# Optimization experiments

Measured on AMD Instinct MI355X. Metric: run time of the kernel, lower is better.

The kernel has to match this reference:

```python
import jax, jax.numpy as jnp
import numpy as np

B = 65536
NUM_INPUTS = 128
H0, H1 = 512, 512
K = 200
MIN_W = 0.001
MIN_H = 0.001
MIN_D = 0.001
EDGE_CONST = float(np.log(np.exp(1.0 - 0.001) - 1.0))  # in-place edge derivative value
LN_EPS = 1e-5


def setup_inputs() -> dict:
    key = jax.random.key(0)
    ks = jax.random.split(key, 10)
    f32 = jnp.float32
    inputs = jax.random.normal(ks[0], (B, NUM_INPUTS), dtype=f32)
    W1 = jax.random.normal(ks[1], (H0, NUM_INPUTS), dtype=f32) / np.sqrt(NUM_INPUTS)
    b1 = jnp.zeros((H0,), f32)
    g1 = jnp.ones((H0,), f32)
    be1 = jnp.zeros((H0,), f32)
    W2 = jax.random.normal(ks[2], (H1, H0), dtype=f32) / np.sqrt(H0)
    b2 = jnp.zeros((H1,), f32)
    g2 = jnp.ones((H1,), f32)
    be2 = jnp.zeros((H1,), f32)
    WV = jax.random.normal(ks[3], (3 * K - 1, H1), dtype=f32) / np.sqrt(H1)
    bV = jnp.zeros((3 * K - 1,), f32)
    Wa = jax.random.normal(ks[4], (1, H1), dtype=f32) / np.sqrt(H1)
    ba = jnp.zeros((1,), f32)
    Wb = jax.random.normal(ks[5], (1, H1), dtype=f32) / np.sqrt(H1)
    bb = jnp.zeros((1,), f32)
    return {"inputs": inputs, "W1": W1, "b1": b1, "g1": g1, "be1": be1,
            "W2": W2, "b2": b2, "g2": g2, "be2": be2,
            "WV": WV, "bV": bV, "Wa": Wa, "ba": ba, "Wb": Wb, "bb": bb}


def _layernorm(x, g, b):
    m = jnp.mean(x, axis=-1, keepdims=True)
    v = jnp.mean(jnp.square(x - m), axis=-1, keepdims=True)
    return (x - m) * jax.lax.rsqrt(v + LN_EPS) * g + b


def _spline_forward(inputs, W1, b1, g1, be1, W2, b2, g2, be2, WV, bV, Wa, ba, Wb, bb):
    x = jax.nn.relu(_layernorm(inputs @ W1.T + b1, g1, be1))
    x = jax.nn.relu(_layernorm(x @ W2.T + b2, g2, be2))
    sp = x @ WV.T + bV                      # [B, 3K-1]
    scale_a = jnp.exp(x @ Wa.T + ba)        # [B, 1]
    scale_b = x @ Wb.T + bb                 # [B, 1]

    Wp = jax.nn.softmax(sp[:, :K], axis=1)
    Hp = jax.nn.softmax(sp[:, K:2 * K], axis=1)
    Dp = sp[:, 2 * K:]                      # [B, K-1]
    Wp = MIN_W + (1.0 - MIN_W * K) * Wp
    Hp = MIN_H + (1.0 - MIN_H * K) * Hp
    Dp = MIN_D + jax.nn.softplus(Dp)
    bsz = inputs.shape[0]
    edge = jnp.full((bsz, 1), EDGE_CONST, dtype=inputs.dtype)
    D = jnp.concatenate([edge, Dp, edge], axis=-1)          # [B, K+1]

    zero = jnp.zeros((bsz, 1), dtype=inputs.dtype)
    cw = jnp.concatenate([zero, jnp.cumsum(Wp, axis=-1)], axis=-1)
    cw = cw.at[:, -1].set(1.0)                              # [B, K+1]
    widths = cw[:, 1:] - cw[:, :-1]                         # [B, K]
    ch = jnp.concatenate([zero, jnp.cumsum(Hp, axis=-1)], axis=-1)
    ch = scale_a * ch + scale_b                             # [B, K+1]
    heights = ch[:, 1:] - ch[:, :-1]                        # [B, K]

    tau = ((jnp.arange(K, dtype=inputs.dtype) + 0.5) / K)   # [K]
    tau = jnp.broadcast_to(tau, (bsz, K))

    # sum(tau >= bins) - 1 == searchsorted(bins, tau, side='right') - 1
    bin_idx = jax.vmap(lambda b, t: jnp.searchsorted(b, t, side='right'))(cw, tau) - 1

    ta = lambda a: jnp.take_along_axis(a, bin_idx, axis=-1)
    in_cw = ta(cw)
    in_w = ta(widths)
    in_ch = ta(ch)
    in_h = ta(heights)
    in_delta = ta(heights / widths)
    d0 = ta(D)
    d1 = ta(D[:, 1:])

    theta = (tau - in_cw) / in_w
    t1mt = theta * (1.0 - theta)
    numer = in_h * (in_delta * jnp.square(theta) + d0 * t1mt)
    denom = in_delta + (d0 + d1 - 2.0 * in_delta) * t1mt
    return in_ch + numer / denom            # [B, K]


def reference(inputs, W1, b1, g1, be1, W2, b2, g2, be2, WV, bV, Wa, ba, Wb, bb):
    return _spline_forward(inputs, W1, b1, g1, be1, W2, b2, g2, be2, WV, bV, Wa, ba, Wb, bb)
```

## Files before the change

### kernel.cpp

```cpp
#include <hip/hip_runtime.h>
#include <stdint.h>

typedef __bf16 bf16;
typedef __bf16 bf16x8 __attribute__((ext_vector_type(8)));
typedef __bf16 bf16x4 __attribute__((ext_vector_type(4)));
typedef float  f32x4  __attribute__((ext_vector_type(4)));
typedef uint32_t u32;

#define BATCH    65536
#define NCAT     640
#define SPSTRIDE 604

#define MFMA __builtin_amdgcn_mfma_f32_16x16x32_bf16
#define FENCE() asm volatile("" ::: "memory")

__device__ __forceinline__ void async16(const void* g, void* l) {
    __builtin_amdgcn_global_load_lds(
        (const u32 __attribute__((address_space(1)))*)g,
        (u32 __attribute__((address_space(3)))*)l,
        16, 0, 0);
}

__global__ __launch_bounds__(256) void prep_kernel(
    const float* W1, const float* W2, const float* WV,
    const float* bV, const float* Wa, const float* ba,
    const float* Wb, const float* bb, const float* inputs,
    bf16* w1b, bf16* w2b, bf16* wcat, float* bcat, bf16* xin)
{
    int idx = blockIdx.x * 256 + threadIdx.x;
    const int n1 = 512 * 128, n2 = 512 * 512, n3 = NCAT * 512;
    const int n5 = BATCH * 128 / 8;
    if (idx < n5) {
        const float4* src = (const float4*)(inputs + idx * 8);
        float4 v0 = src[0], v1 = src[1];
        bf16x8 h;
        h[0]=(bf16)v0.x; h[1]=(bf16)v0.y; h[2]=(bf16)v0.z; h[3]=(bf16)v0.w;
        h[4]=(bf16)v1.x; h[5]=(bf16)v1.y; h[6]=(bf16)v1.z; h[7]=(bf16)v1.w;
        *(bf16x8*)&xin[idx * 8] = h;
        return;
    }
    idx -= n5;
    if (idx < n1) { w1b[idx] = (bf16)W1[idx]; return; }
    idx -= n1;
    if (idx < n2) { w2b[idx] = (bf16)W2[idx]; return; }
    idx -= n2;
    if (idx < n3) {
        int n = idx >> 9, k = idx & 511;
        float v = 0.f;
        if (n < 599)       v = WV[n * 512 + k];
        else if (n == 599) v = Wa[k];
        else if (n == 600) v = Wb[k];
        wcat[idx] = (bf16)v;
        return;
    }
    idx -= n3;
    if (idx < NCAT) {
        float v = 0.f;
        if (idx < 599)       v = bV[idx];
        else if (idx == 599) v = ba[0];
        else if (idx == 600) v = bb[0];
        bcat[idx] = v;
    }
}

template <int KDIM>
__global__ __launch_bounds__(1024, 4) void gemm_ln(
    const bf16* __restrict__ A, const bf16* __restrict__ W,
    const float* __restrict__ bias, const float* __restrict__ gamma,
    const float* __restrict__ beta, bf16* out)
{
    __shared__ __align__(16) char smem[65536];
    __shared__ float Psum[128][4], Psq[128][4];

    const int t = threadIdx.x;
    const int lane = t & 63, wid = t >> 6;
    const int wm = wid >> 2, wn = wid & 3;
    const int l16 = lane & 15, g16 = lane >> 4;
    const long row0 = (long)blockIdx.x * 128;
    constexpr int NT = KDIM / 32;

    const bf16* arow0 = A + (row0 + wm * 32 + l16) * (long)KDIM + g16 * 8;
    const bf16* arow1 = arow0 + 16 * KDIM;

    f32x4 acc[2][8];
#pragma unroll
    for (int a = 0; a < 2; ++a)
#pragma unroll
        for (int b = 0; b < 8; ++b) acc[a][b] = (f32x4){0.f, 0.f, 0.f, 0.f};

    auto stageB = [&](int kt, int bi) {
#pragma unroll
        for (int c = 0; c < 2; ++c) {
            int call = c * 16 + wid;
            int row = call * 16 + (lane >> 2);
            const bf16* src = W + (long)row * KDIM + kt * 32 + (lane & 3) * 8;
            async16(src, smem + bi * 32768 + call * 1024);
        }
    };

    stageB(0, 0);
    FENCE();
    bf16x8 af0 = *(const bf16x8*)(arow0);
    bf16x8 af1 = *(const bf16x8*)(arow1);
    asm volatile("s_waitcnt vmcnt(2)\n\ts_barrier" ::: "memory");

    for (int kt = 0; kt < NT; ++kt) {
        const int bi = kt & 1;
        bf16x8 a0 = af0, a1 = af1;
        if (kt + 1 < NT) {
            stageB(kt + 1, bi ^ 1);
            FENCE();
            af0 = *(const bf16x8*)(arow0 + (kt + 1) * 32);
            af1 = *(const bf16x8*)(arow1 + (kt + 1) * 32);
        }
        const bf16* Bb = (const bf16*)(smem + bi * 32768);
#pragma unroll
        for (int fn = 0; fn < 8; ++fn) {
            bf16x8 bv = *(const bf16x8*)(Bb + (wn * 128 + fn * 16 + l16) * 32 + g16 * 8);
            acc[0][fn] = MFMA(a0, bv, acc[0][fn], 0, 0, 0);
            acc[1][fn] = MFMA(a1, bv, acc[1][fn], 0, 0, 0);
        }
        if (kt + 1 < NT)
            asm volatile("s_waitcnt vmcnt(2)\n\ts_barrier" ::: "memory");
    }

    float gv[8], bev[8];
#pragma unroll
    for (int fn = 0; fn < 8; ++fn) {
        int col = wn * 128 + fn * 16 + l16;
        float bv = bias[col];
        gv[fn] = gamma[col]; bev[fn] = beta[col];
#pragma unroll
        for (int fm = 0; fm < 2; ++fm)
#pragma unroll
            for (int i = 0; i < 4; ++i) acc[fm][fn][i] += bv;
    }
#pragma unroll
    for (int fm = 0; fm < 2; ++fm)
#pragma unroll
        for (int i = 0; i < 4; ++i) {
            float s = 0.f, q = 0.f;
#pragma unroll
            for (int fn = 0; fn < 8; ++fn) { float v = acc[fm][fn][i]; s += v; q += v * v; }
#pragma unroll
            for (int m = 1; m < 16; m <<= 1) { s += __shfl_xor(s, m); q += __shfl_xor(q, m); }
            if (l16 == 0) {
                int lr = wm * 32 + fm * 16 + g16 * 4 + i;
                Psum[lr][wn] = s; Psq[lr][wn] = q;
            }
        }
    __syncthreads();
    float mmean[2][4], mrstd[2][4];
#pragma unroll
    for (int fm = 0; fm < 2; ++fm)
#pragma unroll
        for (int i = 0; i < 4; ++i) {
            int lr = wm * 32 + fm * 16 + g16 * 4 + i;
            float s = Psum[lr][0] + Psum[lr][1] + Psum[lr][2] + Psum[lr][3];
            float q = Psq[lr][0] + Psq[lr][1] + Psq[lr][2] + Psq[lr][3];
            float mean = s * (1.f / 512.f);
            float var  = q * (1.f / 512.f) - mean * mean;
            mmean[fm][i] = mean;
            mrstd[fm][i] = rsqrtf(var + 1e-5f);
        }
    bf16* stg = (bf16*)smem;
#pragma unroll
    for (int h = 0; h < 2; ++h) {
        __syncthreads();
#pragma unroll
        for (int fm = 0; fm < 2; ++fm)
#pragma unroll
            for (int i = 0; i < 4; ++i) {
                int lr = wm * 32 + fm * 16 + g16 * 4 + i;
                if ((lr >> 6) != h) continue;
#pragma unroll
                for (int fn = 0; fn < 8; ++fn) {
                    int col = wn * 128 + fn * 16 + l16;
                    float o = (acc[fm][fn][i] - mmean[fm][i]) * mrstd[fm][i] * gv[fn] + bev[fn];
                    stg[(lr & 63) * 512 + col] = (bf16)fmaxf(o, 0.f);
                }
            }
        __syncthreads();
#pragma unroll
        for (int it = 0; it < 4; ++it) {
            int idx = it * 1024 + t;
            *(bf16x8*)&out[(row0 + h * 64 + (idx >> 6)) * 512 + (idx & 63) * 8] =
                *(const bf16x8*)&stg[idx * 8];
        }
    }
}

__global__ __launch_bounds__(1024, 4) void gemm_cat(
    const bf16* __restrict__ A, const bf16* __restrict__ W,
    const float* __restrict__ bcat, bf16* __restrict__ sp, float* __restrict__ ab)
{
    __shared__ __align__(16) char smem[81920];

    const int t = threadIdx.x;
    const int lane = t & 63, wid = t >> 6;
    const int wm = wid >> 2, wn = wid & 3;
    const int l16 = lane & 15, g16 = lane >> 4;
    const long row0 = (long)blockIdx.x * 128;

    const bf16* arow0 = A + (row0 + wm * 32 + l16) * 512 + g16 * 8;
    const bf16* arow1 = arow0 + 16 * 512;

    f32x4 acc[2][10];
#pragma unroll
    for (int a = 0; a < 2; ++a)
#pragma unroll
        for (int b = 0; b < 10; ++b) acc[a][b] = (f32x4){0.f, 0.f, 0.f, 0.f};

    auto stageB = [&](int kt, int bi) {
#pragma unroll
        for (int c = 0; c < 3; ++c) {
            int call = c * 16 + wid;
            if (call < 40) {
                int row = call * 16 + (lane >> 2);
                const bf16* src = W + (long)row * 512 + kt * 32 + (lane & 3) * 8;
                async16(src, smem + bi * 40960 + call * 1024);
            }
        }
    };

    stageB(0, 0);
    FENCE();
    bf16x8 af0 = *(const bf16x8*)(arow0);
    bf16x8 af1 = *(const bf16x8*)(arow1);
    asm volatile("s_waitcnt vmcnt(2)\n\ts_barrier" ::: "memory");

    for (int kt = 0; kt < 16; ++kt) {
        const int bi = kt & 1;
        bf16x8 a0 = af0, a1 = af1;
        if (kt + 1 < 16) {
            stageB(kt + 1, bi ^ 1);
            FENCE();
            af0 = *(const bf16x8*)(arow0 + (kt + 1) * 32);
            af1 = *(const bf16x8*)(arow1 + (kt + 1) * 32);
        }
        const bf16* Bb = (const bf16*)(smem + bi * 40960);
#pragma unroll
        for (int fn = 0; fn < 10; ++fn) {
            bf16x8 bv = *(const bf16x8*)(Bb + (wn * 160 + fn * 16 + l16) * 32 + g16 * 8);
            acc[0][fn] = MFMA(a0, bv, acc[0][fn], 0, 0, 0);
            acc[1][fn] = MFMA(a1, bv, acc[1][fn], 0, 0, 0);
        }
        if (kt + 1 < 16)
            asm volatile("s_waitcnt vmcnt(2)\n\ts_barrier" ::: "memory");
    }
    __syncthreads();

    float bv[10];
#pragma unroll
    for (int fn = 0; fn < 10; ++fn) bv[fn] = bcat[wn * 160 + fn * 16 + l16];

#pragma unroll
    for (int fn = 0; fn < 10; ++fn) {
        int col = wn * 160 + fn * 16 + l16;
        if (col == 599 || col == 600) {
#pragma unroll
            for (int fm = 0; fm < 2; ++fm)
#pragma unroll
                for (int i = 0; i < 4; ++i) {
                    int lr = wm * 32 + fm * 16 + g16 * 4 + i;
                    ab[(row0 + lr) * 2 + (col - 599)] = acc[fm][fn][i] + bv[fn];
                }
        }
    }

    bf16* stg = (bf16*)smem;
#pragma unroll
    for (int h = 0; h < 2; ++h) {
        __syncthreads();
#pragma unroll
        for (int fn = 0; fn < 10; ++fn) {
            int col = wn * 160 + fn * 16 + l16;
            if (col >= SPSTRIDE) continue;
#pragma unroll
            for (int fm = 0; fm < 2; ++fm)
#pragma unroll
                for (int i = 0; i < 4; ++i) {
                    int lr = wm * 32 + fm * 16 + g16 * 4 + i;
                    if ((lr >> 6) != h) continue;
                    stg[(lr & 63) * SPSTRIDE + col] = (bf16)(acc[fm][fn][i] + bv[fn]);
                }
        }
        __syncthreads();
#pragma unroll
        for (int it = 0; it < 10; ++it) {
            int c = it * 1024 + t;
            if (c < 64 * 151) {
                int r = c / 151, k = c - r * 151;
                *(uint64_t*)&sp[(row0 + h * 64 + r) * SPSTRIDE + k * 4] =
                    *(const uint64_t*)&stg[r * SPSTRIDE + k * 4];
            }
        }
    }
}

__global__ __launch_bounds__(256) void spline_kernel(
    const bf16* __restrict__ sp, const float* __restrict__ ab, float* __restrict__ out)
{
    __shared__ float S[4][816];
    const int t = threadIdx.x;
    const int lane = t & 63, wid = t >> 6;
    const long row = (long)blockIdx.x * 4 + wid;
    const bf16* spr = sp + row * SPSTRIDE;
    const bool act = lane < 50;
    const float EC = 0.53974247f;
    float* cw = &S[wid][0];
    float* ch = &S[wid][204];
    float* dd = &S[wid][408];
    int*   bx = (int*)&S[wid][612];

    const float sa = __expf(ab[row * 2 + 0]);
    const float sb = ab[row * 2 + 1];

    auto rng = [](float x) -> int {
        int v = (int)ceilf(fmaf(200.f, x, -0.5f));
        return v < 0 ? 0 : (v > 200 ? 200 : v);
    };

    float p0, p1, p2, p3;
    {
        float x0, x1, x2v, x3;
        if (act) {
            bf16x4 v = *(const bf16x4*)&spr[4 * lane];
            x0 = (float)v[0]; x1 = (float)v[1]; x2v = (float)v[2]; x3 = (float)v[3];
        } else { x0 = x1 = x2v = x3 = -1e30f; }
        float m = fmaxf(fmaxf(x0, x1), fmaxf(x2v, x3));
#pragma unroll
        for (int d = 1; d < 64; d <<= 1) m = fmaxf(m, __shfl_xor(m, d));
        float e0 = act ? __expf(x0 - m) : 0.f;
        float e1 = act ? __expf(x1 - m) : 0.f;
        float e2 = act ? __expf(x2v - m) : 0.f;
        float e3 = act ? __expf(x3 - m) : 0.f;
        float s = e0 + e1 + e2 + e3;
#pragma unroll
        for (int d = 1; d < 64; d <<= 1) s += __shfl_xor(s, d);
        float inv = 0.8f / s;
        p0 = act ? fmaf(e0, inv, 0.001f) : 0.f;
        p1 = act ? fmaf(e1, inv, 0.001f) : 0.f;
        p2 = act ? fmaf(e2, inv, 0.001f) : 0.f;
        p3 = act ? fmaf(e3, inv, 0.001f) : 0.f;
    }
    float c0 = p0, c1 = c0 + p1, c2 = c1 + p2, c3 = c2 + p3;
    float run = c3, ts = run;
#pragma unroll
    for (int d = 1; d < 64; d <<= 1) { float u = __shfl_up(ts, d); if (lane >= d) ts += u; }
    float excl  = ts - run;
    float nexcl = __shfl_down(excl, 1);
    float cwl0 = excl, cwl1 = excl + c0, cwl2 = excl + c1, cwl3 = excl + c2;

    float hp0, hp1, hp2, hp3;
    {
        float x0, x1, x2v, x3;
        if (act) {
            bf16x4 v = *(const bf16x4*)&spr[200 + 4 * lane];
            x0 = (float)v[0]; x1 = (float)v[1]; x2v = (float)v[2]; x3 = (float)v[3];
        } else { x0 = x1 = x2v = x3 = -1e30f; }
        float m = fmaxf(fmaxf(x0, x1), fmaxf(x2v, x3));
#pragma unroll
        for (int d = 1; d < 64; d <<= 1) m = fmaxf(m, __shfl_xor(m, d));
        float e0 = act ? __expf(x0 - m) : 0.f;
        float e1 = act ? __expf(x1 - m) : 0.f;
        float e2 = act ? __expf(x2v - m) : 0.f;
        float e3 = act ? __expf(x3 - m) : 0.f;
        float s = e0 + e1 + e2 + e3;
#pragma unroll
        for (int d = 1; d < 64; d <<= 1) s += __shfl_xor(s, d);
        float inv = 0.8f / s;
        hp0 = act ? fmaf(e0, inv, 0.001f) : 0.f;
        hp1 = act ? fmaf(e1, inv, 0.001f) : 0.f;
        hp2 = act ? fmaf(e2, inv, 0.001f) : 0.f;
        hp3 = act ? fmaf(e3, inv, 0.001f) : 0.f;
    }
    float hc0 = hp0, hc1 = hc0 + hp1, hc2 = hc1 + hp2, hc3 = hc2 + hp3;
    float hrun = hc3, hts = hrun;
#pragma unroll
    for (int d = 1; d < 64; d <<= 1) { float u = __shfl_up(hts, d); if (lane >= d) hts += u; }
    float hexcl = hts - hrun;
    float ch0 = fmaf(sa, hexcl, sb);
    float ch1 = fmaf(sa, hexcl + hc0, sb);
    float ch2 = fmaf(sa, hexcl + hc1, sb);
    float ch3 = fmaf(sa, hexcl + hc2, sb);

    float dv0, dv1, dv2, dv3;
    {
        float x0 = 0.f, x1 = 0.f, x2v = 0.f, x3 = 0.f;
        if (act) {
            bf16x4 v = *(const bf16x4*)&spr[400 + 4 * lane];
            x0 = (float)v[0]; x1 = (float)v[1]; x2v = (float)v[2]; x3 = (float)v[3];
        }
        auto spls = [](float x) {
            return fmaxf(x, 0.f) + __logf(1.f + __expf(-fabsf(x))) + 0.001f;
        };
        dv0 = spls(x0); dv1 = spls(x1); dv2 = spls(x2v); dv3 = spls(x3);
    }
    if (lane == 49) dv3 = EC;
    float dprev = __shfl_up(dv3, 1);
    if (lane == 0) dprev = EC;

    if (act) {
        *(f32x4*)&cw[4 * lane] = (f32x4){cwl0, cwl1, cwl2, cwl3};
        *(f32x4*)&ch[4 * lane] = (f32x4){ch0, ch1, ch2, ch3};
        *(f32x4*)&dd[4 * lane] = (f32x4){dprev, dv0, dv1, dv2};
    }
    if (lane == 49) {
        cw[200] = 1.0f;
        ch[200] = fmaf(sa, hts, sb);
        dd[200] = EC;
    }

    if (act) {
        int b0 = rng(cwl0), b1 = rng(cwl1), b2 = rng(cwl2), b3 = rng(cwl3);
        int b4 = (lane == 49) ? 200 : rng(nexcl);
        for (int j = b0; j < b1; ++j) bx[j] = 4 * lane;
        for (int j = b1; j < b2; ++j) bx[j] = 4 * lane + 1;
        for (int j = b2; j < b3; ++j) bx[j] = 4 * lane + 2;
        for (int j = b3; j < b4; ++j) bx[j] = 4 * lane + 3;
    }
    asm volatile("s_waitcnt lgkmcnt(0)" ::: "memory");

    if (act) {
        float* orow = out + (size_t)row * 200;
#pragma unroll
        for (int k = 0; k < 4; ++k) {
            int j = lane + 50 * k;
            int b = bx[j];
            float wl = cw[b], wr = cw[b + 1];
            float hl = ch[b], hr = ch[b + 1];
            float d0 = dd[b], d1 = dd[b + 1];
            float tau = ((float)j + 0.5f) * (1.f / 200.f);
            float w = wr - wl, h = hr - hl;
            float invw = 1.f / w;
            float delta = h * invw;
            float th = (tau - wl) * invw;
            float t1 = th * (1.f - th);
            float numer = h * fmaf(delta * th, th, d0 * t1);
            float denom = fmaf(d0 + d1 - 2.f * delta, t1, delta);
            orow[j] = hl + numer / denom;
        }
    }
}

extern "C" void kernel_launch(void* const* d_in, const int* in_sizes, int n_in,
                              void* d_out, int out_size, void* d_ws, size_t ws_size,
                              hipStream_t stream)
{
    const float* inputs = (const float*)d_in[0];
    const float* W1  = (const float*)d_in[1];
    const float* b1  = (const float*)d_in[2];
    const float* g1  = (const float*)d_in[3];
    const float* be1 = (const float*)d_in[4];
    const float* W2  = (const float*)d_in[5];
    const float* b2  = (const float*)d_in[6];
    const float* g2  = (const float*)d_in[7];
    const float* be2 = (const float*)d_in[8];
    const float* WV  = (const float*)d_in[9];
    const float* bV  = (const float*)d_in[10];
    const float* Wa  = (const float*)d_in[11];
    const float* ba  = (const float*)d_in[12];
    const float* Wb  = (const float*)d_in[13];
    const float* bb  = (const float*)d_in[14];
    float* out = (float*)d_out;

    char* ws = (char*)d_ws;
    bf16*  w1b  = (bf16*) (ws + 0);
    bf16*  w2b  = (bf16*) (ws + 131072);
    bf16*  wcat = (bf16*) (ws + 655360);
    float* bcat = (float*)(ws + 1310720);
    float* ab   = (float*)(ws + 1313280);
    bf16*  x    = (bf16*) (ws + 2097152);
    bf16*  spb  = (bf16*) (ws + 69206016);
    bf16*  xin  = (bf16*) (ws + 69206016);

    const int preptot = BATCH * 128 / 8 + 512 * 128 + 512 * 512 + NCAT * 512 + NCAT;
    prep_kernel<<<(preptot + 255) / 256, 256, 0, stream>>>(
        W1, W2, WV, bV, Wa, ba, Wb, bb, inputs, w1b, w2b, wcat, bcat, xin);

    gemm_ln<128><<<BATCH / 128, 1024, 0, stream>>>(xin, w1b, b1, g1, be1, x);
    gemm_ln<512><<<BATCH / 128, 1024, 0, stream>>>(x,   w2b, b2, g2, be2, x);
    gemm_cat<<<BATCH / 128, 1024, 0, stream>>>(x, wcat, bcat, spb, ab);
    spline_kernel<<<BATCH / 4, 256, 0, stream>>>(spb, ab, out);
}
```

Measured before the change: 248.8 us.

## Retile GEMM warps to 2x8 grid with 4x4 MFMA fragments and setprio

Both GEMM kernels change the warp layout from 4x4 (32 rows x 128/160 cols per warp) to 2x8 (64 rows x 64/80 cols per warp). Each B fragment read from LDS now feeds four MFMAs instead of two, which lowers LDS read traffic per MFMA, while each warp issues twice as many A global loads. The MFMA block is wrapped in s_setprio, the LN partial-sum arrays grow to 8 column groups, and the sp row stride is padded from 604 to 608 so the copy-out is more regular. The spline kernel must read sp with the same stride; it uses SPSTRIDE, so it stays consistent.

```diff
diff --git a/kernel.cpp b/kernel.cpp
--- a/kernel.cpp
+++ b/kernel.cpp
@@ -9,7 +9,7 @@
 
 #define BATCH    65536
 #define NCAT     640
-#define SPSTRIDE 604
+#define SPSTRIDE 608
 
 #define MFMA __builtin_amdgcn_mfma_f32_16x16x32_bf16
 #define FENCE() asm volatile("" ::: "memory")
@@ -70,23 +70,22 @@
     const float* __restrict__ beta, bf16* out)
 {
     __shared__ __align__(16) char smem[65536];
-    __shared__ float Psum[128][4], Psq[128][4];
+    __shared__ float Psum[128][8], Psq[128][8];
 
     const int t = threadIdx.x;
     const int lane = t & 63, wid = t >> 6;
-    const int wm = wid >> 2, wn = wid & 3;
+    const int wm = wid >> 3, wn = wid & 7;
     const int l16 = lane & 15, g16 = lane >> 4;
     const long row0 = (long)blockIdx.x * 128;
     constexpr int NT = KDIM / 32;
 
-    const bf16* arow0 = A + (row0 + wm * 32 + l16) * (long)KDIM + g16 * 8;
-    const bf16* arow1 = arow0 + 16 * KDIM;
-
-    f32x4 acc[2][8];
-#pragma unroll
-    for (int a = 0; a < 2; ++a)
-#pragma unroll
-        for (int b = 0; b < 8; ++b) acc[a][b] = (f32x4){0.f, 0.f, 0.f, 0.f};
+    const bf16* arow = A + (row0 + wm * 64 + l16) * (long)KDIM + g16 * 8;
+
+    f32x4 acc[4][4];
+#pragma unroll
+    for (int a = 0; a < 4; ++a)
+#pragma unroll
+        for (int b = 0; b < 4; ++b) acc[a][b] = (f32x4){0.f, 0.f, 0.f, 0.f};
 
     auto stageB = [&](int kt, int bi) {
 #pragma unroll
@@ -98,66 +97,73 @@
         }
     };
 
+    bf16x8 af[4];
     stageB(0, 0);
     FENCE();
-    bf16x8 af0 = *(const bf16x8*)(arow0);
-    bf16x8 af1 = *(const bf16x8*)(arow1);
-    asm volatile("s_waitcnt vmcnt(2)\n\ts_barrier" ::: "memory");
+#pragma unroll
+    for (int fm = 0; fm < 4; ++fm) af[fm] = *(const bf16x8*)(arow + fm * 16 * KDIM);
+    asm volatile("s_waitcnt vmcnt(4)\n\ts_barrier" ::: "memory");
 
     for (int kt = 0; kt < NT; ++kt) {
         const int bi = kt & 1;
-        bf16x8 a0 = af0, a1 = af1;
+        bf16x8 a0 = af[0], a1 = af[1], a2 = af[2], a3 = af[3];
         if (kt + 1 < NT) {
             stageB(kt + 1, bi ^ 1);
             FENCE();
-            af0 = *(const bf16x8*)(arow0 + (kt + 1) * 32);
-            af1 = *(const bf16x8*)(arow1 + (kt + 1) * 32);
+            const bf16* ap = arow + (kt + 1) * 32;
+#pragma unroll
+            for (int fm = 0; fm < 4; ++fm) af[fm] = *(const bf16x8*)(ap + fm * 16 * KDIM);
         }
         const bf16* Bb = (const bf16*)(smem + bi * 32768);
-#pragma unroll
-        for (int fn = 0; fn < 8; ++fn) {
-            bf16x8 bv = *(const bf16x8*)(Bb + (wn * 128 + fn * 16 + l16) * 32 + g16 * 8);
+        __builtin_amdgcn_s_setprio(1);
+#pragma unroll
+        for (int fn = 0; fn < 4; ++fn) {
+            bf16x8 bv = *(const bf16x8*)(Bb + (wn * 64 + fn * 16 + l16) * 32 + g16 * 8);
             acc[0][fn] = MFMA(a0, bv, acc[0][fn], 0, 0, 0);
             acc[1][fn] = MFMA(a1, bv, acc[1][fn], 0, 0, 0);
-        }
+            acc[2][fn] = MFMA(a2, bv, acc[2][fn], 0, 0, 0);
+            acc[3][fn] = MFMA(a3, bv, acc[3][fn], 0, 0, 0);
+        }
+        __builtin_amdgcn_s_setprio(0);
         if (kt + 1 < NT)
-            asm volatile("s_waitcnt vmcnt(2)\n\ts_barrier" ::: "memory");
-    }
-
-    float gv[8], bev[8];
-#pragma unroll
-    for (int fn = 0; fn < 8; ++fn) {
-        int col = wn * 128 + fn * 16 + l16;
+            asm volatile("s_waitcnt vmcnt(4)\n\ts_barrier" ::: "memory");
+    }
+
+    float gv[4], bev[4];
+#pragma unroll
+    for (int fn = 0; fn < 4; ++fn) {
+        int col = wn * 64 + fn * 16 + l16;
         float bv = bias[col];
         gv[fn] = gamma[col]; bev[fn] = beta[col];
 #pragma unroll
-        for (int fm = 0; fm < 2; ++fm)
+        for (int fm = 0; fm < 4; ++fm)
 #pragma unroll
             for (int i = 0; i < 4; ++i) acc[fm][fn][i] += bv;
     }
 #pragma unroll
-    for (int fm = 0; fm < 2; ++fm)
+    for (int fm = 0; fm < 4; ++fm)
 #pragma unroll
         for (int i = 0; i < 4; ++i) {
             float s = 0.f, q = 0.f;
 #pragma unroll
-            for (int fn = 0; fn < 8; ++fn) { float v = acc[fm][fn][i]; s += v; q += v * v; }
+            for (int fn = 0; fn < 4; ++fn) { float v = acc[fm][fn][i]; s += v; q += v * v; }
 #pragma unroll
             for (int m = 1; m < 16; m <<= 1) { s += __shfl_xor(s, m); q += __shfl_xor(q, m); }
             if (l16 == 0) {
-                int lr = wm * 32 + fm * 16 + g16 * 4 + i;
+                int lr = wm * 64 + fm * 16 + g16 * 4 + i;
                 Psum[lr][wn] = s; Psq[lr][wn] = q;
             }
         }
     __syncthreads();
-    float mmean[2][4], mrstd[2][4];
-#pragma unroll
-    for (int fm = 0; fm < 2; ++fm)
+    float mmean[4][4], mrstd[4][4];
+#pragma unroll
+    for (int fm = 0; fm < 4; ++fm)
 #pragma unroll
         for (int i = 0; i < 4; ++i) {
-            int lr = wm * 32 + fm * 16 + g16 * 4 + i;
-            float s = Psum[lr][0] + Psum[lr][1] + Psum[lr][2] + Psum[lr][3];
-            float q = Psq[lr][0] + Psq[lr][1] + Psq[lr][2] + Psq[lr][3];
+            int lr = wm * 64 + fm * 16 + g16 * 4 + i;
+            float s = 0.f, q = 0.f;
+#pragma unroll
+            for (int g = 0; g < 8; ++g) { s += Psum[lr][g]; q += Psq[lr][g]; }
             float mean = s * (1.f / 512.f);
             float var  = q * (1.f / 512.f) - mean * mean;
             mmean[fm][i] = mean;
@@ -167,19 +173,20 @@
 #pragma unroll
     for (int h = 0; h < 2; ++h) {
         __syncthreads();
-#pragma unroll
-        for (int fm = 0; fm < 2; ++fm)
-#pragma unroll
-            for (int i = 0; i < 4; ++i) {
-                int lr = wm * 32 + fm * 16 + g16 * 4 + i;
-                if ((lr >> 6) != h) continue;
-#pragma unroll
-                for (int fn = 0; fn < 8; ++fn) {
-                    int col = wn * 128 + fn * 16 + l16;
-                    float o = (acc[fm][fn][i] - mmean[fm][i]) * mrstd[fm][i] * gv[fn] + bev[fn];
-                    stg[(lr & 63) * 512 + col] = (bf16)fmaxf(o, 0.f);
+        if (wm == h) {
+#pragma unroll
+            for (int fm = 0; fm < 4; ++fm)
+#pragma unroll
+                for (int i = 0; i < 4; ++i) {
+                    int lr = fm * 16 + g16 * 4 + i;
+#pragma unroll
+                    for (int fn = 0; fn < 4; ++fn) {
+                        int col = wn * 64 + fn * 16 + l16;
+                        float o = (acc[fm][fn][i] - mmean[fm][i]) * mrstd[fm][i] * gv[fn] + bev[fn];
+                        stg[lr * 512 + col] = (bf16)fmaxf(o, 0.f);
+                    }
                 }
-            }
+        }
         __syncthreads();
 #pragma unroll
         for (int it = 0; it < 4; ++it) {
@@ -198,18 +205,17 @@
 
     const int t = threadIdx.x;
     const int lane = t & 63, wid = t >> 6;
-    const int wm = wid >> 2, wn = wid & 3;
+    const int wm = wid >> 3, wn = wid & 7;
     const int l16 = lane & 15, g16 = lane >> 4;
     const long row0 = (long)blockIdx.x * 128;
 
-    const bf16* arow0 = A + (row0 + wm * 32 + l16) * 512 + g16 * 8;
-    const bf16* arow1 = arow0 + 16 * 512;
-
-    f32x4 acc[2][10];
-#pragma unroll
-    for (int a = 0; a < 2; ++a)
-#pragma unroll
-        for (int b = 0; b < 10; ++b) acc[a][b] = (f32x4){0.f, 0.f, 0.f, 0.f};
+    const bf16* arow = A + (row0 + wm * 64 + l16) * 512 + g16 * 8;
+
+    f32x4 acc[4][5];
+#pragma unroll
+    for (int a = 0; a < 4; ++a)
+#pragma unroll
+        for (int b = 0; b < 5; ++b) acc[a][b] = (f32x4){0.f, 0.f, 0.f, 0.f};
 
     auto stageB = [&](int kt, int bi) {
 #pragma unroll
@@ -223,46 +229,52 @@
         }
     };
 
+    bf16x8 af[4];
     stageB(0, 0);
     FENCE();
-    bf16x8 af0 = *(const bf16x8*)(arow0);
-    bf16x8 af1 = *(const bf16x8*)(arow1);
-    asm volatile("s_waitcnt vmcnt(2)\n\ts_barrier" ::: "memory");
+#pragma unroll
+    for (int fm = 0; fm < 4; ++fm) af[fm] = *(const bf16x8*)(arow + fm * 16 * 512);
+    asm volatile("s_waitcnt vmcnt(4)\n\ts_barrier" ::: "memory");
 
     for (int kt = 0; kt < 16; ++kt) {
         const int bi = kt & 1;
-        bf16x8 a0 = af0, a1 = af1;
+        bf16x8 a0 = af[0], a1 = af[1], a2 = af[2], a3 = af[3];
         if (kt + 1 < 16) {
             stageB(kt + 1, bi ^ 1);
             FENCE();
-            af0 = *(const bf16x8*)(arow0 + (kt + 1) * 32);
-            af1 = *(const bf16x8*)(arow1 + (kt + 1) * 32);
+            const bf16* ap = arow + (kt + 1) * 32;
+#pragma unroll
+            for (int fm = 0; fm < 4; ++fm) af[fm] = *(const bf16x8*)(ap + fm * 16 * 512);
         }
         const bf16* Bb = (const bf16*)(smem + bi * 40960);
-#pragma unroll
-        for (int fn = 0; fn < 10; ++fn) {
-            bf16x8 bv = *(const bf16x8*)(Bb + (wn * 160 + fn * 16 + l16) * 32 + g16 * 8);
+        __builtin_amdgcn_s_setprio(1);
+#pragma unroll
+        for (int fn = 0; fn < 5; ++fn) {
+            bf16x8 bv = *(const bf16x8*)(Bb + (wn * 80 + fn * 16 + l16) * 32 + g16 * 8);
             acc[0][fn] = MFMA(a0, bv, acc[0][fn], 0, 0, 0);
             acc[1][fn] = MFMA(a1, bv, acc[1][fn], 0, 0, 0);
-        }
+            acc[2][fn] = MFMA(a2, bv, acc[2][fn], 0, 0, 0);
+            acc[3][fn] = MFMA(a3, bv, acc[3][fn], 0, 0, 0);
+        }
+        __builtin_amdgcn_s_setprio(0);
         if (kt + 1 < 16)
-            asm volatile("s_waitcnt vmcnt(2)\n\ts_barrier" ::: "memory");
+            asm volatile("s_waitcnt vmcnt(4)\n\ts_barrier" ::: "memory");
     }
     __syncthreads();
 
-    float bv[10];
-#pragma unroll
-    for (int fn = 0; fn < 10; ++fn) bv[fn] = bcat[wn * 160 + fn * 16 + l16];
-
-#pragma unroll
-    for (int fn = 0; fn < 10; ++fn) {
-        int col = wn * 160 + fn * 16 + l16;
+    float bv[5];
+#pragma unroll
+    for (int fn = 0; fn < 5; ++fn) bv[fn] = bcat[wn * 80 + fn * 16 + l16];
+
+#pragma unroll
+    for (int fn = 0; fn < 5; ++fn) {
+        int col = wn * 80 + fn * 16 + l16;
         if (col == 599 || col == 600) {
 #pragma unroll
-            for (int fm = 0; fm < 2; ++fm)
+            for (int fm = 0; fm < 4; ++fm)
 #pragma unroll
                 for (int i = 0; i < 4; ++i) {
-                    int lr = wm * 32 + fm * 16 + g16 * 4 + i;
+                    int lr = wm * 64 + fm * 16 + g16 * 4 + i;
                     ab[(row0 + lr) * 2 + (col - 599)] = acc[fm][fn][i] + bv[fn];
                 }
         }
@@ -272,25 +284,27 @@
 #pragma unroll
     for (int h = 0; h < 2; ++h) {
         __syncthreads();
-#pragma unroll
-        for (int fn = 0; fn < 10; ++fn) {
-            int col = wn * 160 + fn * 16 + l16;
-            if (col >= SPSTRIDE) continue;
-#pragma unroll
-            for (int fm = 0; fm < 2; ++fm)
-#pragma unroll
-                for (int i = 0; i < 4; ++i) {
-                    int lr = wm * 32 + fm * 16 + g16 * 4 + i;
-                    if ((lr >> 6) != h) continue;
-                    stg[(lr & 63) * SPSTRIDE + col] = (bf16)(acc[fm][fn][i] + bv[fn]);
+        if (wm == h) {
+#pragma unroll
+            for (int fn = 0; fn < 5; ++fn) {
+                int col = wn * 80 + fn * 16 + l16;
+                if (col < SPSTRIDE) {
+#pragma unroll
+                    for (int fm = 0; fm < 4; ++fm)
+#pragma unroll
+                        for (int i = 0; i < 4; ++i) {
+                            int lr = fm * 16 + g16 * 4 + i;
+                            stg[lr * SPSTRIDE + col] = (bf16)(acc[fm][fn][i] + bv[fn]);
+                        }
                 }
+            }
         }
         __syncthreads();
 #pragma unroll
         for (int it = 0; it < 10; ++it) {
             int c = it * 1024 + t;
-            if (c < 64 * 151) {
-                int r = c / 151, k = c - r * 151;
+            if (c < 64 * 152) {
+                int r = c >> 7 >> 0; r = c / 152; int k = c - r * 152;
                 *(uint64_t*)&sp[(row0 + h * 64 + r) * SPSTRIDE + k * 4] =
                     *(const uint64_t*)&stg[r * SPSTRIDE + k * 4];
             }
```

New measurement: 359.9 us. +44.7%, slower.

## Split concat GEMM across two column halves and triple-buffer weight tiles

Applied to the files above, without the earlier changes.

The concatenated head GEMM now launches twice as many blocks, each computing half of the 640 output columns, which halves accumulator registers and shared memory per block. The B-tile staging goes from double to triple buffering with a prefetch distance of two, and the sp row stride widens to 608 so the two halves can write aligned segments. The aim is higher occupancy and better latency hiding in this GEMM. The cost is that each A tile is read twice from global memory and block scheduling overhead doubles.

```diff
diff --git a/kernel.cpp b/kernel.cpp
--- a/kernel.cpp
+++ b/kernel.cpp
@@ -9,7 +9,7 @@
 
 #define BATCH    65536
 #define NCAT     640
-#define SPSTRIDE 604
+#define SPSTRIDE 608
 
 #define MFMA __builtin_amdgcn_mfma_f32_16x16x32_bf16
 #define FENCE() asm volatile("" ::: "memory")
@@ -194,77 +194,83 @@
     const bf16* __restrict__ A, const bf16* __restrict__ W,
     const float* __restrict__ bcat, bf16* __restrict__ sp, float* __restrict__ ab)
 {
-    __shared__ __align__(16) char smem[81920];
+    __shared__ __align__(16) char smem[61440];
 
     const int t = threadIdx.x;
     const int lane = t & 63, wid = t >> 6;
     const int wm = wid >> 2, wn = wid & 3;
     const int l16 = lane & 15, g16 = lane >> 4;
-    const long row0 = (long)blockIdx.x * 128;
+    const int nh  = blockIdx.x & 1;
+    const long row0 = (long)(blockIdx.x >> 1) * 128;
 
     const bf16* arow0 = A + (row0 + wm * 32 + l16) * 512 + g16 * 8;
     const bf16* arow1 = arow0 + 16 * 512;
 
-    f32x4 acc[2][10];
+    f32x4 acc[2][5];
 #pragma unroll
     for (int a = 0; a < 2; ++a)
 #pragma unroll
-        for (int b = 0; b < 10; ++b) acc[a][b] = (f32x4){0.f, 0.f, 0.f, 0.f};
+        for (int b = 0; b < 5; ++b) acc[a][b] = (f32x4){0.f, 0.f, 0.f, 0.f};
 
     auto stageB = [&](int kt, int bi) {
 #pragma unroll
-        for (int c = 0; c < 3; ++c) {
+        for (int c = 0; c < 2; ++c) {
             int call = c * 16 + wid;
-            if (call < 40) {
-                int row = call * 16 + (lane >> 2);
+            if (call < 20) {
+                int row = nh * 320 + call * 16 + (lane >> 2);
                 const bf16* src = W + (long)row * 512 + kt * 32 + (lane & 3) * 8;
-                async16(src, smem + bi * 40960 + call * 1024);
+                async16(src, smem + bi * 20480 + call * 1024);
             }
         }
     };
 
     stageB(0, 0);
+    stageB(1, 1);
     FENCE();
     bf16x8 af0 = *(const bf16x8*)(arow0);
     bf16x8 af1 = *(const bf16x8*)(arow1);
-    asm volatile("s_waitcnt vmcnt(2)\n\ts_barrier" ::: "memory");
-
+    asm volatile("s_waitcnt vmcnt(3)\n\ts_barrier" ::: "memory");
+
+#pragma unroll
     for (int kt = 0; kt < 16; ++kt) {
-        const int bi = kt & 1;
+        const int cur = kt % 3;
         bf16x8 a0 = af0, a1 = af1;
+        if (kt + 2 < 16) { stageB(kt + 2, (kt + 2) % 3); FENCE(); }
         if (kt + 1 < 16) {
-            stageB(kt + 1, bi ^ 1);
-            FENCE();
             af0 = *(const bf16x8*)(arow0 + (kt + 1) * 32);
             af1 = *(const bf16x8*)(arow1 + (kt + 1) * 32);
         }
-        const bf16* Bb = (const bf16*)(smem + bi * 40960);
-#pragma unroll
-        for (int fn = 0; fn < 10; ++fn) {
-            bf16x8 bv = *(const bf16x8*)(Bb + (wn * 160 + fn * 16 + l16) * 32 + g16 * 8);
+        const bf16* Bb = (const bf16*)(smem + cur * 20480);
+#pragma unroll
+        for (int fn = 0; fn < 5; ++fn) {
+            bf16x8 bv = *(const bf16x8*)(Bb + (wn * 80 + fn * 16 + l16) * 32 + g16 * 8);
             acc[0][fn] = MFMA(a0, bv, acc[0][fn], 0, 0, 0);
             acc[1][fn] = MFMA(a1, bv, acc[1][fn], 0, 0, 0);
         }
-        if (kt + 1 < 16)
+        if (kt + 2 < 16)
+            asm volatile("s_waitcnt vmcnt(3)\n\ts_barrier" ::: "memory");
+        else if (kt + 1 < 16)
             asm volatile("s_waitcnt vmcnt(2)\n\ts_barrier" ::: "memory");
     }
     __syncthreads();
 
-    float bv[10];
-#pragma unroll
-    for (int fn = 0; fn < 10; ++fn) bv[fn] = bcat[wn * 160 + fn * 16 + l16];
-
-#pragma unroll
-    for (int fn = 0; fn < 10; ++fn) {
-        int col = wn * 160 + fn * 16 + l16;
-        if (col == 599 || col == 600) {
-#pragma unroll
-            for (int fm = 0; fm < 2; ++fm)
-#pragma unroll
-                for (int i = 0; i < 4; ++i) {
-                    int lr = wm * 32 + fm * 16 + g16 * 4 + i;
-                    ab[(row0 + lr) * 2 + (col - 599)] = acc[fm][fn][i] + bv[fn];
-                }
+    float bv[5];
+#pragma unroll
+    for (int fn = 0; fn < 5; ++fn) bv[fn] = bcat[nh * 320 + wn * 80 + fn * 16 + l16];
+
+    if (nh == 1) {
+#pragma unroll
+        for (int fn = 0; fn < 5; ++fn) {
+            int col = 320 + wn * 80 + fn * 16 + l16;
+            if (col == 599 || col == 600) {
+#pragma unroll
+                for (int fm = 0; fm < 2; ++fm)
+#pragma unroll
+                    for (int i = 0; i < 4; ++i) {
+                        int lr = wm * 32 + fm * 16 + g16 * 4 + i;
+                        ab[(row0 + lr) * 2 + (col - 599)] = acc[fm][fn][i] + bv[fn];
+                    }
+            }
         }
     }
 
@@ -272,27 +278,31 @@
 #pragma unroll
     for (int h = 0; h < 2; ++h) {
         __syncthreads();
-#pragma unroll
-        for (int fn = 0; fn < 10; ++fn) {
-            int col = wn * 160 + fn * 16 + l16;
-            if (col >= SPSTRIDE) continue;
-#pragma unroll
-            for (int fm = 0; fm < 2; ++fm)
-#pragma unroll
-                for (int i = 0; i < 4; ++i) {
-                    int lr = wm * 32 + fm * 16 + g16 * 4 + i;
-                    if ((lr >> 6) != h) continue;
-                    stg[(lr & 63) * SPSTRIDE + col] = (bf16)(acc[fm][fn][i] + bv[fn]);
-                }
+        if ((wm >> 1) == h) {
+#pragma unroll
+            for (int fn = 0; fn < 5; ++fn) {
+                int lcol = wn * 80 + fn * 16 + l16;
+#pragma unroll
+                for (int fm = 0; fm < 2; ++fm)
+#pragma unroll
+                    for (int i = 0; i < 4; ++i) {
+                        int lr = (wm & 1) * 32 + fm * 16 + g16 * 4 + i;
+                        stg[lr * 320 + lcol] = (bf16)(acc[fm][fn][i] + bv[fn]);
+                    }
+            }
         }
         __syncthreads();
-#pragma unroll
-        for (int it = 0; it < 10; ++it) {
-            int c = it * 1024 + t;
-            if (c < 64 * 151) {
-                int r = c / 151, k = c - r * 151;
+        if (nh == 0) {
+            for (int c = t; c < 64 * 80; c += 1024) {
+                int r = c / 80, k = c - r * 80;
                 *(uint64_t*)&sp[(row0 + h * 64 + r) * SPSTRIDE + k * 4] =
-                    *(const uint64_t*)&stg[r * SPSTRIDE + k * 4];
+                    *(const uint64_t*)&stg[r * 320 + k * 4];
+            }
+        } else {
+            for (int c = t; c < 64 * 72; c += 1024) {
+                int r = c / 72, k = c - r * 72;
+                *(uint64_t*)&sp[(row0 + h * 64 + r) * SPSTRIDE + 320 + k * 4] =
+                    *(const uint64_t*)&stg[r * 320 + k * 4];
             }
         }
     }
@@ -481,6 +491,6 @@
 
     gemm_ln<128><<<BATCH / 128, 1024, 0, stream>>>(xin, w1b, b1, g1, be1, x);
     gemm_ln<512><<<BATCH / 128, 1024, 0, stream>>>(x,   w2b, b2, g2, be2, x);
-    gemm_cat<<<BATCH / 128, 1024, 0, stream>>>(x, wcat, bcat, spb, ab);
+    gemm_cat<<<(BATCH / 128) * 2, 1024, 0, stream>>>(x, wcat, bcat, spb, ab);
     spline_kernel<<<BATCH / 4, 256, 0, stream>>>(spb, ab, out);
 }
```

New measurement: 263.2 us (median of 2 runs). 5.8% more time.
